# Kernel tuning notes

Measured on AMD Instinct MI355X. Metric: run time of the kernel, lower is better.

Reference implementation:

```python
import jax, jax.numpy as jnp
import numpy as np

NUM_QUANTIZERS = 8
CODEBOOK_SIZE = 1024
DIM = 64
B, N = 8, 8192


def setup_inputs() -> dict:
    key = jax.random.key(0)
    kx, kc = jax.random.split(key)
    x = jax.random.normal(kx, (B, N, DIM), dtype=jnp.float32)
    # one codebook per quantizer stage (shared_codebook=False)
    codebooks = jax.random.normal(kc, (NUM_QUANTIZERS, CODEBOOK_SIZE, DIM), dtype=jnp.float32)
    return {"x": x, "codebooks": codebooks}


def reference(x, codebooks):
    """Residual VQ: sequential nearest-codebook lookup with residual subtraction.

    x:         [b, n, d]
    codebooks: [Q, K, d]
    returns quantized_out: [b, n, d]
    """

    def step(carry, cb):
        residual, qout = carry                       # [b,n,d], [b,n,d]
        # squared euclidean distances, [b,n,K]
        r_sq = jnp.sum(residual * residual, axis=-1, keepdims=True)
        c_sq = jnp.sum(cb * cb, axis=-1)             # [K]
        dots = jnp.einsum('bnd,kd->bnk', residual, cb)
        dist = r_sq - 2.0 * dots + c_sq              # [b,n,K]
        idx = jnp.argmin(dist, axis=-1)              # [b,n]
        quant = cb[idx]                              # [b,n,d] gather
        # straight-through estimator (VectorQuantize forward)
        quant_st = residual + jax.lax.stop_gradient(quant - residual)
        new_residual = residual - jax.lax.stop_gradient(quant)
        return (new_residual, qout + quant_st), idx

    init = (x, jnp.zeros_like(x))
    (residual, quantized_out), all_indices = jax.lax.scan(step, init, codebooks)
    return quantized_out
```

## Files before the change

### kernel.cpp

```cpp
#include <hip/hip_runtime.h>

#define NQ 8
#define KCODES 1024
#define D 64
#define CHUNK 128
#define NCHUNK 8
#define TPB 512
#define TOKPB 128

using short8 = __attribute__((ext_vector_type(8))) short;
using f32x4  = __attribute__((ext_vector_type(4))) float;

static __device__ __forceinline__ unsigned bf16_rne_bits(float f) {
    unsigned u = __float_as_uint(f);
    return (u + 0x7fffu + ((u >> 16) & 1u)) >> 16;
}

__global__ __launch_bounds__(256) void prep_cb(const float* __restrict__ cb,
                                               int4* __restrict__ ws_cb) {
    int id = blockIdx.x * 256 + threadIdx.x;
    int slot = id & 2047;
    int qc = id >> 11;
    int q = qc >> 3, ch = qc & 7;
    int plane = slot >> 7, n_rel = slot & 127;
    int g = plane & 3, kt = (plane >> 2) & 1, term = plane >> 3;
    int n = ch * CHUNK + n_rel;
    const float* src = cb + ((size_t)(q * KCODES + n)) * D + kt * 32 + g * 8;
    union { short s[8]; int4 v; } u;
    #pragma unroll
    for (int j = 0; j < 8; ++j) {
        float f = src[j];
        unsigned hb = bf16_rne_bits(f);
        if (term == 0) {
            u.s[j] = (short)hb;
        } else {
            float lo = f - __uint_as_float(hb << 16);
            u.s[j] = (short)bf16_rne_bits(lo);
        }
    }
    ws_cb[id] = u.v;
}

__global__ __launch_bounds__(256) void prep_csq(const float* __restrict__ cb,
                                                float* __restrict__ ws_csq,
                                                float* __restrict__ ws_csqh) {
    int id = blockIdx.x * 256 + threadIdx.x;
    const float* c = cb + (size_t)id * D;
    float s0 = 0.f, s1 = 0.f, s2 = 0.f, s3 = 0.f;
    #pragma unroll
    for (int j = 0; j < 16; ++j) {
        s0 = fmaf(c[4*j+0], c[4*j+0], s0);
        s1 = fmaf(c[4*j+1], c[4*j+1], s1);
        s2 = fmaf(c[4*j+2], c[4*j+2], s2);
        s3 = fmaf(c[4*j+3], c[4*j+3], s3);
    }
    float cs = (s0 + s1) + (s2 + s3);
    ws_csq[id]  = cs;
    ws_csqh[id] = -0.5f * cs;
}

__global__ __launch_bounds__(TPB, 4) void rvq_mfma(
    const float* __restrict__ x,
    const float* __restrict__ cb,
    const int4* __restrict__ ws_cb,
    const float* __restrict__ ws_csq,
    const float* __restrict__ ws_csqh,
    float* __restrict__ out)
{
    __shared__ __align__(16) char smem[TOKPB * 68 * 4];
    int4*  lds_cb    = (int4*)smem;
    float* lds_resid = (float*)smem;
    __shared__ float lds_csqh[CHUNK];
    __shared__ int2  lds_cand[TOKPB];
    __shared__ int   lds_pick[TOKPB];

    const int tid  = threadIdx.x;
    const int lane = tid & 63;
    const int wave = tid >> 6;
    const int g    = lane >> 4;
    const int c    = lane & 15;
    const int ltok = wave * 16 + c;
    const int tok  = blockIdx.x * TOKPB + ltok;

    const float4* xp = (const float4*)(x + (size_t)tok * D);
    float4 rv0 = xp[g*2], rv1 = xp[g*2+1], rv2 = xp[8+g*2], rv3 = xp[8+g*2+1];

    const char* bp = smem + (c << 4) + (g << 11);

    for (int q = 0; q < NQ; ++q) {
        short8 ah0, al0, ah1, al1;
        {
            const float* fv0 = (const float*)&rv0;
            const float* fv1 = (const float*)&rv1;
            const float* fv2 = (const float*)&rv2;
            const float* fv3 = (const float*)&rv3;
            #pragma unroll
            for (int j = 0; j < 4; ++j) {
                float a = fv0[j], b = fv1[j], e = fv2[j], f = fv3[j];
                unsigned ha = bf16_rne_bits(a);
                unsigned hbv = bf16_rne_bits(b);
                unsigned he = bf16_rne_bits(e);
                unsigned hf = bf16_rne_bits(f);
                ah0[j]   = (short)ha;  ah0[4+j] = (short)hbv;
                ah1[j]   = (short)he;  ah1[4+j] = (short)hf;
                al0[j]   = (short)bf16_rne_bits(a - __uint_as_float(ha  << 16));
                al0[4+j] = (short)bf16_rne_bits(b - __uint_as_float(hbv << 16));
                al1[j]   = (short)bf16_rne_bits(e - __uint_as_float(he  << 16));
                al1[4+j] = (short)bf16_rne_bits(f - __uint_as_float(hf  << 16));
            }
        }

        float d1[4], d2[4]; int i1[4], i2[4];
        #pragma unroll
        for (int r = 0; r < 4; ++r) { d1[r] = -3.0e38f; d2[r] = -3.0e38f; i1[r] = 0; i2[r] = 0; }

        for (int ch = 0; ch < NCHUNK; ++ch) {
            __syncthreads();
            {
                const int4* src = ws_cb + (size_t)(q * NCHUNK + ch) * 2048;
                #pragma unroll
                for (int t = 0; t < 4; ++t) lds_cb[tid + t * TPB] = src[tid + t * TPB];
                if (tid < CHUNK) lds_csqh[tid] = ws_csqh[q * KCODES + ch * CHUNK + tid];
            }
            __syncthreads();

            const int code_base = ch * CHUNK + c;
            #pragma unroll
            for (int tile = 0; tile < 8; ++tile) {
                short8 bh0 = *(const short8*)(bp + tile * 256);
                short8 bh1 = *(const short8*)(bp + 8192  + tile * 256);
                short8 bl0 = *(const short8*)(bp + 16384 + tile * 256);
                short8 bl1 = *(const short8*)(bp + 24576 + tile * 256);
                const float sd = lds_csqh[tile * 16 + c];
                f32x4 acc = {sd, sd, sd, sd};
                acc = __builtin_amdgcn_mfma_f32_16x16x32_bf16(ah0, bh0, acc, 0, 0, 0);
                acc = __builtin_amdgcn_mfma_f32_16x16x32_bf16(ah1, bh1, acc, 0, 0, 0);
                acc = __builtin_amdgcn_mfma_f32_16x16x32_bf16(al0, bh0, acc, 0, 0, 0);
                acc = __builtin_amdgcn_mfma_f32_16x16x32_bf16(ah0, bl0, acc, 0, 0, 0);
                acc = __builtin_amdgcn_mfma_f32_16x16x32_bf16(al1, bh1, acc, 0, 0, 0);
                acc = __builtin_amdgcn_mfma_f32_16x16x32_bf16(ah1, bl1, acc, 0, 0, 0);
                acc = __builtin_amdgcn_mfma_f32_16x16x32_bf16(al0, bl0, acc, 0, 0, 0);
                acc = __builtin_amdgcn_mfma_f32_16x16x32_bf16(al1, bl1, acc, 0, 0, 0);

                const int codev = code_base + tile * 16;
                #pragma unroll
                for (int r = 0; r < 4; ++r) {
                    float v = acc[r];
                    bool gt1 = v > d1[r];
                    bool gt2 = v > d2[r];
                    float vm = fminf(v, d1[r]);
                    d1[r] = fmaxf(v, d1[r]);
                    d2[r] = gt2 ? vm : d2[r];
                    i2[r] = gt1 ? i1[r] : (gt2 ? codev : i2[r]);
                    i1[r] = gt1 ? codev : i1[r];
                }
            }
        }

        #pragma unroll
        for (int s = 1; s <= 8; s <<= 1) {
            #pragma unroll
            for (int r = 0; r < 4; ++r) {
                float od1 = __shfl_xor(d1[r], s);
                int   oi1 = __shfl_xor(i1[r], s);
                float od2 = __shfl_xor(d2[r], s);
                int   oi2 = __shfl_xor(i2[r], s);
                bool keep = (d1[r] > od1) || (d1[r] == od1 && i1[r] < oi1);
                float w1 = keep ? d1[r] : od1;  int wi1 = keep ? i1[r] : oi1;
                float l1 = keep ? od1 : d1[r];  int li1 = keep ? oi1 : i1[r];
                bool bsec = (od2 > d2[r]) || (od2 == d2[r] && oi2 < i2[r]);
                float y  = bsec ? od2 : d2[r];  int yi = bsec ? oi2 : i2[r];
                bool xw  = (l1 > y) || (l1 == y && li1 < yi);
                d2[r] = xw ? l1 : y;  i2[r] = xw ? li1 : yi;
                d1[r] = w1; i1[r] = wi1;
            }
        }

        __syncthreads();
        if (c == 0) {
            #pragma unroll
            for (int r = 0; r < 4; ++r)
                lds_cand[wave * 16 + g * 4 + r] = make_int2(i1[r], i2[r]);
        }
        {
            float* rr = lds_resid + (size_t)ltok * 68;
            *(float4*)(rr + 8*g)      = rv0;
            *(float4*)(rr + 8*g + 4)  = rv1;
            *(float4*)(rr + 32 + 8*g) = rv2;
            *(float4*)(rr + 36 + 8*g) = rv3;
        }
        __syncthreads();

        {
            const int t = (lane >> 1) & 15;
            const int2 cnd = lds_cand[wave * 16 + t];
            const int cd = (lane & 1) ? cnd.y : cnd.x;
            const float4* rrv = (const float4*)(lds_resid + (size_t)(wave * 16 + t) * 68);
            const float4* cpv = (const float4*)(cb + ((size_t)(q * KCODES + cd)) * D);
            float ax = 0.f, ay = 0.f, az = 0.f, aw = 0.f;
            #pragma unroll
            for (int j = 0; j < 16; ++j) {
                float4 rv = rrv[j];
                float4 cv = cpv[j];
                ax = fmaf(rv.x, cv.x, ax);
                ay = fmaf(rv.y, cv.y, ay);
                az = fmaf(rv.z, cv.z, az);
                aw = fmaf(rv.w, cv.w, aw);
            }
            float dot = (ax + ay) + (az + aw);
            float dd = fmaf(dot, -2.0f, ws_csq[q * KCODES + cd]);
            float od = __shfl_xor(dd, 1);
            float dA = (lane & 1) ? od : dd;
            float dB = (lane & 1) ? dd : od;
            int lo  = cnd.x < cnd.y ? cnd.x : cnd.y;
            int hi  = cnd.x < cnd.y ? cnd.y : cnd.x;
            float dlo = cnd.x < cnd.y ? dA : dB;
            float dhi = cnd.x < cnd.y ? dB : dA;
            int pick = (dhi < dlo) ? hi : lo;
            if (lane < 32 && (lane & 1) == 0) lds_pick[wave * 16 + t] = pick;
        }
        __syncthreads();
        const int ifin = lds_pick[ltok];

        {
            const float4* cp = (const float4*)(cb + ((size_t)(q * KCODES + ifin)) * D);
            float4 c0 = cp[g*2], c1 = cp[g*2+1], c2 = cp[8+g*2], c3 = cp[8+g*2+1];
            rv0.x -= c0.x; rv0.y -= c0.y; rv0.z -= c0.z; rv0.w -= c0.w;
            rv1.x -= c1.x; rv1.y -= c1.y; rv1.z -= c1.z; rv1.w -= c1.w;
            rv2.x -= c2.x; rv2.y -= c2.y; rv2.z -= c2.z; rv2.w -= c2.w;
            rv3.x -= c3.x; rv3.y -= c3.y; rv3.z -= c3.z; rv3.w -= c3.w;
        }
    }

    {
        float4* op = (float4*)(out + (size_t)tok * D);
        float4 xv0 = xp[g*2], xv1 = xp[g*2+1], xv2 = xp[8+g*2], xv3 = xp[8+g*2+1];
        float4 o0, o1, o2, o3;
        o0.x = xv0.x - rv0.x; o0.y = xv0.y - rv0.y; o0.z = xv0.z - rv0.z; o0.w = xv0.w - rv0.w;
        o1.x = xv1.x - rv1.x; o1.y = xv1.y - rv1.y; o1.z = xv1.z - rv1.z; o1.w = xv1.w - rv1.w;
        o2.x = xv2.x - rv2.x; o2.y = xv2.y - rv2.y; o2.z = xv2.z - rv2.z; o2.w = xv2.w - rv2.w;
        o3.x = xv3.x - rv3.x; o3.y = xv3.y - rv3.y; o3.z = xv3.z - rv3.z; o3.w = xv3.w - rv3.w;
        op[g*2] = o0; op[g*2+1] = o1; op[8+g*2] = o2; op[8+g*2+1] = o3;
    }
}

extern "C" void kernel_launch(void* const* d_in, const int* in_sizes, int n_in,
                              void* d_out, int out_size, void* d_ws, size_t ws_size,
                              hipStream_t stream) {
    const float* x  = (const float*)d_in[0];
    const float* cb = (const float*)d_in[1];
    float* out = (float*)d_out;

    int4*  ws_cb   = (int4*)d_ws;
    float* ws_csq  = (float*)((char*)d_ws + (size_t)2 * 1024 * 1024);
    float* ws_csqh = ws_csq + 8192;

    prep_cb <<<512, 256, 0, stream>>>(cb, ws_cb);
    prep_csq<<< 32, 256, 0, stream>>>(cb, ws_csq, ws_csqh);

    const int n_tokens = in_sizes[0] / D;
    const int grid = n_tokens / TOKPB;
    rvq_mfma<<<grid, TPB, 0, stream>>>(x, cb, ws_cb, ws_csq, ws_csqh, out);
}
```

Baseline: 421.3 us.

## Split codebook scan across wave pairs and use direct global-to-LDS loads

Halves tokens per block and assigns two waves to each 16-token group, each scanning half of every codebook chunk, then merges their top-2 candidates through LDS before exact rescoring. Codebook staging switches to global_load_lds so data goes straight into shared memory without passing through registers. The top-2 update is rewritten with fewer selects. This raises block count and parallelism per token but doubles total codebook staging traffic per token and adds a cross-wave merge step.

```diff
diff --git a/kernel.cpp b/kernel.cpp
--- a/kernel.cpp
+++ b/kernel.cpp
@@ -6,10 +6,13 @@
 #define CHUNK 128
 #define NCHUNK 8
 #define TPB 512
-#define TOKPB 128
+#define TOKPB 64
 
 using short8 = __attribute__((ext_vector_type(8))) short;
 using f32x4  = __attribute__((ext_vector_type(4))) float;
+
+#define GLOBAL_AS __attribute__((address_space(1)))
+#define LDS_AS    __attribute__((address_space(3)))
 
 static __device__ __forceinline__ unsigned bf16_rne_bits(float f) {
     unsigned u = __float_as_uint(f);
@@ -59,7 +62,7 @@
     ws_csqh[id] = -0.5f * cs;
 }
 
-__global__ __launch_bounds__(TPB, 4) void rvq_mfma(
+__global__ __launch_bounds__(TPB, 8) void rvq_mfma(
     const float* __restrict__ x,
     const float* __restrict__ cb,
     const int4* __restrict__ ws_cb,
@@ -67,25 +70,26 @@
     const float* __restrict__ ws_csqh,
     float* __restrict__ out)
 {
-    __shared__ __align__(16) char smem[TOKPB * 68 * 4];
-    int4*  lds_cb    = (int4*)smem;
+    __shared__ __align__(16) char smem[32768];
     float* lds_resid = (float*)smem;
     __shared__ float lds_csqh[CHUNK];
-    __shared__ int2  lds_cand[TOKPB];
+    __shared__ int4  lds_cand[8 * 16];
     __shared__ int   lds_pick[TOKPB];
 
-    const int tid  = threadIdx.x;
-    const int lane = tid & 63;
-    const int wave = tid >> 6;
-    const int g    = lane >> 4;
-    const int c    = lane & 15;
-    const int ltok = wave * 16 + c;
-    const int tok  = blockIdx.x * TOKPB + ltok;
+    const int tid   = threadIdx.x;
+    const int lane  = tid & 63;
+    const int wave  = tid >> 6;
+    const int group = wave >> 1;
+    const int half  = wave & 1;
+    const int g     = lane >> 4;
+    const int c     = lane & 15;
+    const int ltok  = group * 16 + c;
+    const int tok   = blockIdx.x * TOKPB + ltok;
 
     const float4* xp = (const float4*)(x + (size_t)tok * D);
     float4 rv0 = xp[g*2], rv1 = xp[g*2+1], rv2 = xp[8+g*2], rv3 = xp[8+g*2+1];
 
-    const char* bp = smem + (c << 4) + (g << 11);
+    const char* bp = smem + (c << 4) + (g << 11) + (half << 10);
 
     for (int q = 0; q < NQ; ++q) {
         short8 ah0, al0, ah1, al1;
@@ -117,21 +121,30 @@
         for (int ch = 0; ch < NCHUNK; ++ch) {
             __syncthreads();
             {
-                const int4* src = ws_cb + (size_t)(q * NCHUNK + ch) * 2048;
+                const int4* src = ws_cb + (size_t)(q * NCHUNK + ch) * 2048 + tid;
+                LDS_AS char* ldst = (LDS_AS char*)(smem) + tid * 16;
                 #pragma unroll
-                for (int t = 0; t < 4; ++t) lds_cb[tid + t * TPB] = src[tid + t * TPB];
-                if (tid < CHUNK) lds_csqh[tid] = ws_csqh[q * KCODES + ch * CHUNK + tid];
+                for (int t = 0; t < 4; ++t) {
+                    __builtin_amdgcn_global_load_lds(
+                        (const GLOBAL_AS unsigned int*)(src + t * TPB),
+                        (LDS_AS unsigned int*)(ldst + t * TPB * 16), 16, 0, 0);
+                }
+                if (tid < CHUNK) {
+                    __builtin_amdgcn_global_load_lds(
+                        (const GLOBAL_AS unsigned int*)(ws_csqh + q * KCODES + ch * CHUNK + tid),
+                        (LDS_AS unsigned int*)(&lds_csqh[tid]), 4, 0, 0);
+                }
             }
             __syncthreads();
 
-            const int code_base = ch * CHUNK + c;
-            #pragma unroll
-            for (int tile = 0; tile < 8; ++tile) {
-                short8 bh0 = *(const short8*)(bp + tile * 256);
-                short8 bh1 = *(const short8*)(bp + 8192  + tile * 256);
-                short8 bl0 = *(const short8*)(bp + 16384 + tile * 256);
-                short8 bl1 = *(const short8*)(bp + 24576 + tile * 256);
-                const float sd = lds_csqh[tile * 16 + c];
+            const int code_base = ch * CHUNK + half * 64 + c;
+            #pragma unroll
+            for (int tt = 0; tt < 4; ++tt) {
+                short8 bh0 = *(const short8*)(bp + tt * 256);
+                short8 bh1 = *(const short8*)(bp + 8192  + tt * 256);
+                short8 bl0 = *(const short8*)(bp + 16384 + tt * 256);
+                short8 bl1 = *(const short8*)(bp + 24576 + tt * 256);
+                const float sd = lds_csqh[half * 64 + tt * 16 + c];
                 f32x4 acc = {sd, sd, sd, sd};
                 acc = __builtin_amdgcn_mfma_f32_16x16x32_bf16(ah0, bh0, acc, 0, 0, 0);
                 acc = __builtin_amdgcn_mfma_f32_16x16x32_bf16(ah1, bh1, acc, 0, 0, 0);
@@ -142,16 +155,16 @@
                 acc = __builtin_amdgcn_mfma_f32_16x16x32_bf16(al0, bl0, acc, 0, 0, 0);
                 acc = __builtin_amdgcn_mfma_f32_16x16x32_bf16(al1, bl1, acc, 0, 0, 0);
 
-                const int codev = code_base + tile * 16;
+                const int codev = code_base + tt * 16;
                 #pragma unroll
                 for (int r = 0; r < 4; ++r) {
                     float v = acc[r];
                     bool gt1 = v > d1[r];
                     bool gt2 = v > d2[r];
-                    float vm = fminf(v, d1[r]);
+                    float nd2 = fmaxf(fminf(d1[r], v), d2[r]);
                     d1[r] = fmaxf(v, d1[r]);
-                    d2[r] = gt2 ? vm : d2[r];
-                    i2[r] = gt1 ? i1[r] : (gt2 ? codev : i2[r]);
+                    d2[r] = nd2;
+                    i2[r] = gt2 ? (gt1 ? i1[r] : codev) : i2[r];
                     i1[r] = gt1 ? codev : i1[r];
                 }
             }
@@ -180,9 +193,10 @@
         if (c == 0) {
             #pragma unroll
             for (int r = 0; r < 4; ++r)
-                lds_cand[wave * 16 + g * 4 + r] = make_int2(i1[r], i2[r]);
-        }
-        {
+                lds_cand[(group * 2 + half) * 16 + g * 4 + r] =
+                    make_int4(__float_as_int(d1[r]), i1[r], __float_as_int(d2[r]), i2[r]);
+        }
+        if (half == 0) {
             float* rr = lds_resid + (size_t)ltok * 68;
             *(float4*)(rr + 8*g)      = rv0;
             *(float4*)(rr + 8*g + 4)  = rv1;
@@ -191,11 +205,24 @@
         }
         __syncthreads();
 
-        {
-            const int t = (lane >> 1) & 15;
-            const int2 cnd = lds_cand[wave * 16 + t];
-            const int cd = (lane & 1) ? cnd.y : cnd.x;
-            const float4* rrv = (const float4*)(lds_resid + (size_t)(wave * 16 + t) * 68);
+        if (half == 0) {
+            const int t   = (lane >> 1) & 15;
+            const int sel = lane & 1;
+            const int4 A = lds_cand[(group * 2 + 0) * 16 + t];
+            const int4 B = lds_cand[(group * 2 + 1) * 16 + t];
+            float a1 = __int_as_float(A.x), a2 = __int_as_float(A.z);
+            float b1 = __int_as_float(B.x), b2 = __int_as_float(B.z);
+            int ai1 = A.y, ai2 = A.w, bi1 = B.y, bi2 = B.w;
+            bool keep = (a1 > b1) || (a1 == b1 && ai1 < bi1);
+            float m1 = keep ? a1 : b1;  int mi1 = keep ? ai1 : bi1;
+            float l1 = keep ? b1 : a1;  int li1 = keep ? bi1 : ai1;
+            float s2 = keep ? a2 : b2;  int si2 = keep ? ai2 : bi2;
+            bool xw = (l1 > s2) || (l1 == s2 && li1 < si2);
+            float m2 = xw ? l1 : s2;    int mi2 = xw ? li1 : si2;
+            (void)m1; (void)m2;
+
+            const int cd = sel ? mi2 : mi1;
+            const float4* rrv = (const float4*)(lds_resid + (size_t)(group * 16 + t) * 68);
             const float4* cpv = (const float4*)(cb + ((size_t)(q * KCODES + cd)) * D);
             float ax = 0.f, ay = 0.f, az = 0.f, aw = 0.f;
             #pragma unroll
@@ -210,14 +237,14 @@
             float dot = (ax + ay) + (az + aw);
             float dd = fmaf(dot, -2.0f, ws_csq[q * KCODES + cd]);
             float od = __shfl_xor(dd, 1);
-            float dA = (lane & 1) ? od : dd;
-            float dB = (lane & 1) ? dd : od;
-            int lo  = cnd.x < cnd.y ? cnd.x : cnd.y;
-            int hi  = cnd.x < cnd.y ? cnd.y : cnd.x;
-            float dlo = cnd.x < cnd.y ? dA : dB;
-            float dhi = cnd.x < cnd.y ? dB : dA;
+            float dA = sel ? od : dd;
+            float dB = sel ? dd : od;
+            int lo  = mi1 < mi2 ? mi1 : mi2;
+            int hi  = mi1 < mi2 ? mi2 : mi1;
+            float dlo = mi1 < mi2 ? dA : dB;
+            float dhi = mi1 < mi2 ? dB : dA;
             int pick = (dhi < dlo) ? hi : lo;
-            if (lane < 32 && (lane & 1) == 0) lds_pick[wave * 16 + t] = pick;
+            if (lane < 32 && sel == 0) lds_pick[group * 16 + t] = pick;
         }
         __syncthreads();
         const int ifin = lds_pick[ltok];
@@ -232,7 +259,7 @@
         }
     }
 
-    {
+    if (half == 0) {
         float4* op = (float4*)(out + (size_t)tok * D);
         float4 xv0 = xp[g*2], xv1 = xp[g*2+1], xv2 = xp[8+g*2], xv3 = xp[8+g*2+1];
         float4 o0, o1, o2, o3;
```

Result: slower. 652.8 us (+54.9%).
